# Optimization experiments

Measured on AMD Instinct MI355X. Metric: run time of the kernel, lower is better.

The kernel has to match this reference:

```python
import jax, jax.numpy as jnp
import numpy as np

OFFSETS = jnp.array([[-1, -1], [0, -1], [1, -1], [-1, 0], [0, 0], [1, 0],
                     [-1, 1], [0, 1], [1, 1]], dtype=jnp.float32)  # [9,2]
PIX_STEP = 2.0 / 96.0


def _bilinear_sample(img, gx, gy):
    """Bilinear grid_sample, padding_mode='zeros', align_corners=False.
    img: [B,H,W]; gx, gy: [B,P] in normalized coords [-1,1]. Returns [B,P]."""
    B, H, W = img.shape
    ix = ((gx + 1.0) * W - 1.0) * 0.5  # x indexes width
    iy = ((gy + 1.0) * H - 1.0) * 0.5
    x0f = jnp.floor(ix)
    y0f = jnp.floor(iy)
    wx = ix - x0f
    wy = iy - y0f
    x0 = x0f.astype(jnp.int32)
    y0 = y0f.astype(jnp.int32)
    x1 = x0 + 1
    y1 = y0 + 1
    flat = img.reshape(B, H * W)

    def gather(xi, yi):
        valid = (xi >= 0) & (xi < W) & (yi >= 0) & (yi < H)
        xc = jnp.clip(xi, 0, W - 1)
        yc = jnp.clip(yi, 0, H - 1)
        vals = jnp.take_along_axis(flat, yc * W + xc, axis=1)
        return jnp.where(valid, vals, 0.0)

    v00 = gather(x0, y0)
    v10 = gather(x1, y0)
    v01 = gather(x0, y1)
    v11 = gather(x1, y1)
    return (v00 * (1 - wx) * (1 - wy) + v10 * wx * (1 - wy)
            + v01 * (1 - wx) * wy + v11 * wx * wy)


def setup_inputs() -> dict:
    key = jax.random.key(0)
    k1, k2, k3 = jax.random.split(key, 3)
    B, N, H, W = 256, 16384, 96, 96
    corners = jax.random.uniform(k1, (B, N, 2), dtype=jnp.float32)
    edge_map = jax.random.uniform(k2, (B, 1, H, W), dtype=jnp.float32)
    mask_map = jax.random.uniform(k3, (B, 1, H, W), dtype=jnp.float32)
    return {"corners": corners, "edge_map": edge_map, "mask_map": mask_map}


def reference(corners, edge_map, mask_map):
    B, N, _ = corners.shape
    grid = corners * 2.0 - 1.0  # [B,N,2] (x,y)
    # 9-point neighborhood around each corner: [B,N,9,2]
    neigh = grid[:, :, None, :] + OFFSETS[None, None] * PIX_STEP
    gx = neigh[..., 0].reshape(B, N * 9)
    gy = neigh[..., 1].reshape(B, N * 9)
    sampled_edges = _bilinear_sample(edge_map[:, 0], gx, gy).reshape(B, N, 9)
    best_edge = jnp.max(sampled_edges, axis=-1)  # [B,N]
    edge_align_loss = jnp.mean(1.0 - best_edge)
    sampled_mask = _bilinear_sample(mask_map[:, 0], grid[..., 0], grid[..., 1])  # [B,N]
    mask_align_loss = jnp.mean((sampled_mask - 0.5) ** 2)
    return edge_align_loss + 2.0 * mask_align_loss
```

## Files before the change

kernel.cpp:

```cpp
#include <hip/hip_runtime.h>
#include <hip/hip_fp16.h>

constexpr int Bn = 256;
constexpr int Nn = 16384;
constexpr int Hh = 96;
constexpr int Ww = 96;

constexpr int THREADS = 1024;
constexpr int CHUNKS  = 2;
constexpr int EPS = 100;
constexpr int ESZ = 100 * 100;
constexpr int MPS = 50;
constexpr int MSZ = 100 * 50;
constexpr int PER_THREAD = Nn / CHUNKS / THREADS;

__global__ __launch_bounds__(THREADS, 8)
void geo_kernel(const float* __restrict__ corners,
                const float* __restrict__ edge,
                const float* __restrict__ mask,
                float2* __restrict__ partial)
{
    __shared__ alignas(16) __half2 sE[ESZ];
    __shared__ alignas(16) __half2 sM[MSZ];
    __shared__ float redE[THREADS / 64];
    __shared__ float redM[THREADS / 64];

    const int b     = blockIdx.x >> 1;
    const int chunk = blockIdx.x & 1;
    const int tid   = threadIdx.x;

    const float4* c4 =
        (const float4*)(corners + (size_t)b * Nn * 2 + (size_t)chunk * (Nn / CHUNKS) * 2);
    float4 cc[4];
#pragma unroll
    for (int k = 0; k < 4; ++k)
        cc[k] = c4[k * THREADS + tid];

    {
        const __half2 z2 = __float22half2_rn(make_float2(0.f, 0.f));
        if (tid < 400) sE[(tid < 200) ? tid : (9600 + tid)] = z2;
        if (tid < 288) {
            int r = tid / 3;
            int k = tid - 3 * r;
            int c = (k == 0) ? 0 : (97 + k);
            sE[(r + 2) * EPS + c] = z2;
        }
        if (tid < 200) sM[(tid < 100) ? tid : (4800 + tid)] = z2;
        if (tid < 192) {
            int r = tid >> 1;
            int c = (tid & 1) ? 49 : 0;
            sM[(r + 2) * MPS + c] = z2;
        }
    }

    {
        const float* ebase = edge + (size_t)b * Hh * Ww;
        const float* mbase = mask + (size_t)b * Hh * Ww;
        for (int i = tid; i < Hh * (Ww / 2); i += THREADS) {
            int r = i / (Ww / 2);
            int j = i - r * (Ww / 2);
            const float* erow = ebase + r * Ww;
            float2 ae = *(const float2*)(erow + 2 * j);
            float ne = (2 * j + 2 < Ww) ? erow[2 * j + 2] : 0.f;
            int base = (r + 2) * EPS + 2 * j + 2;
            sE[base]     = __float22half2_rn(make_float2(ae.x, ae.y));
            sE[base + 1] = __float22half2_rn(make_float2(ae.y, ne));
            if (j == 0)
                sE[(r + 2) * EPS + 1] = __float22half2_rn(make_float2(0.f, ae.x));
            float2 am = *(const float2*)(mbase + r * Ww + 2 * j);
            sM[(r + 2) * MPS + 1 + j] = __float22half2_rn(make_float2(am.x, am.y));
        }
    }
    __syncthreads();

    float eAcc = 0.f, mAcc = 0.f;
#pragma unroll
    for (int jj = 0; jj < PER_THREAD; ++jj) {
        float cx = (jj & 1) ? ((jj & 2) ? cc[jj >> 1].z : cc[jj >> 1].z)
                            : cc[jj >> 1].x;
        float cy;
        if (jj & 1) { cx = cc[jj >> 1].z; cy = cc[jj >> 1].w; }
        else        { cx = cc[jj >> 1].x; cy = cc[jj >> 1].y; }
        float ix = fmaf(cx, 96.f, -0.5f);
        float iy = fmaf(cy, 96.f, -0.5f);
        float x0f = floorf(ix), y0f = floorf(iy);
        float wx = ix - x0f, wy = iy - y0f;
        int x0 = (int)x0f, y0 = (int)y0f;

        int cb = (y0 + 1) * EPS + (x0 + 1);
        __half2 e00 = sE[cb],           e01 = sE[cb + 2];
        __half2 e10 = sE[cb + EPS],     e11 = sE[cb + EPS + 2];
        __half2 e20 = sE[cb + 2 * EPS], e21 = sE[cb + 2 * EPS + 2];
        __half2 e30 = sE[cb + 3 * EPS], e31 = sE[cb + 3 * EPS + 2];

        int e0  = (x0 + 2) >> 1;
        int odd = x0 & 1;
        int mb  = (y0 + 2) * MPS + e0;
        __half2 ma_lo = sM[mb],       ma_hi = sM[mb + 1];
        __half2 mc_lo = sM[mb + MPS], mc_hi = sM[mb + MPS + 1];

        float2 r00 = __half22float2(e00), r01 = __half22float2(e01);
        float2 r10 = __half22float2(e10), r11 = __half22float2(e11);
        float2 r20 = __half22float2(e20), r21 = __half22float2(e21);
        float2 r30 = __half22float2(e30), r31 = __half22float2(e31);

        float h[4][3];
        h[0][0] = fmaf(wx, r00.y - r00.x, r00.x);
        h[0][1] = fmaf(wx, r01.x - r00.y, r00.y);
        h[0][2] = fmaf(wx, r01.y - r01.x, r01.x);
        h[1][0] = fmaf(wx, r10.y - r10.x, r10.x);
        h[1][1] = fmaf(wx, r11.x - r10.y, r10.y);
        h[1][2] = fmaf(wx, r11.y - r11.x, r11.x);
        h[2][0] = fmaf(wx, r20.y - r20.x, r20.x);
        h[2][1] = fmaf(wx, r21.x - r20.y, r20.y);
        h[2][2] = fmaf(wx, r21.y - r21.x, r21.x);
        h[3][0] = fmaf(wx, r30.y - r30.x, r30.x);
        h[3][1] = fmaf(wx, r31.x - r30.y, r30.y);
        h[3][2] = fmaf(wx, r31.y - r31.x, r31.x);

        float best = fmaf(wy, h[1][0] - h[0][0], h[0][0]);
#pragma unroll
        for (int r = 0; r < 3; ++r) {
#pragma unroll
            for (int k = 0; k < 3; ++k) {
                if (r == 0 && k == 0) continue;
                float s = fmaf(wy, h[r + 1][k] - h[r][k], h[r][k]);
                best = fmaxf(best, s);
            }
        }
        eAcc += best;

        float2 qa = __half22float2(ma_lo), qb = __half22float2(ma_hi);
        float2 qc = __half22float2(mc_lo), qd = __half22float2(mc_hi);
        float l0 = odd ? qa.y : qa.x;
        float r0 = odd ? qb.x : qa.y;
        float l1 = odd ? qc.y : qc.x;
        float r1 = odd ? qd.x : qc.y;
        float t = fmaf(wx, r0 - l0, l0);
        float u = fmaf(wx, r1 - l1, l1);
        float m = fmaf(wy, u - t, t);
        float d = m - 0.5f;
        mAcc = fmaf(d, d, mAcc);
    }

#pragma unroll
    for (int off = 32; off > 0; off >>= 1) {
        eAcc += __shfl_xor(eAcc, off);
        mAcc += __shfl_xor(mAcc, off);
    }
    const int wv = tid >> 6;
    const int ln = tid & 63;
    if (ln == 0) { redE[wv] = eAcc; redM[wv] = mAcc; }
    __syncthreads();

    if (tid == 0) {
        float e = 0.f, m = 0.f;
#pragma unroll
        for (int w = 0; w < THREADS / 64; ++w) { e += redE[w]; m += redM[w]; }
        partial[blockIdx.x] = make_float2(e, m);
    }
}

__global__ __launch_bounds__(512)
void geo_reduce(const float2* __restrict__ partial, float* __restrict__ out)
{
    __shared__ double rE[8];
    __shared__ double rM[8];
    const int tid = threadIdx.x;
    float2 p = partial[tid];
    double e = (double)p.x, m = (double)p.y;
#pragma unroll
    for (int off = 32; off > 0; off >>= 1) {
        e += __shfl_xor(e, off);
        m += __shfl_xor(m, off);
    }
    if ((tid & 63) == 0) { rE[tid >> 6] = e; rM[tid >> 6] = m; }
    __syncthreads();
    if (tid == 0) {
        double se = 0.0, sm = 0.0;
#pragma unroll
        for (int w = 0; w < 8; ++w) { se += rE[w]; sm += rM[w]; }
        const double inv = 1.0 / (double)((long long)Bn * (long long)Nn);
        double edge_loss = 1.0 - se * inv;
        double mask_loss = sm * inv;
        out[0] = (float)(edge_loss + 2.0 * mask_loss);
    }
}

extern "C" void kernel_launch(void* const* d_in, const int* in_sizes, int n_in,
                              void* d_out, int out_size, void* d_ws, size_t ws_size,
                              hipStream_t stream)
{
    const float* corners = (const float*)d_in[0];
    const float* edge    = (const float*)d_in[1];
    const float* mask    = (const float*)d_in[2];
    float* out      = (float*)d_out;
    float2* partial = (float2*)d_ws;

    geo_kernel<<<Bn * CHUNKS, THREADS, 0, stream>>>(corners, edge, mask, partial);
    geo_reduce<<<1, 512, 0, stream>>>(partial, out);
}
```

Baseline: 28.97 us.

## Halve shared-memory tile via non-duplicated half2 layout and smaller blocks

Replaces the duplicated shifted-pair edge layout (100-wide half2 rows) with a plain packed half2 layout (51 words per row), rebuilding odd-aligned pairs with shift/or funnel operations at sample time. This cuts LDS per block from about 60KB to about 40KB. It also switches to 512-thread blocks with 4 chunks per image, so more blocks can be resident and tile staging overlaps with compute. Corner loads are moved after the barrier and split into two phases. The cost is extra ALU work per sample, staging the image tile twice as often across blocks, and a larger final reduction.

```diff
diff --git a/kernel.cpp b/kernel.cpp
--- a/kernel.cpp
+++ b/kernel.cpp
@@ -6,13 +6,24 @@
 constexpr int Hh = 96;
 constexpr int Ww = 96;
 
-constexpr int THREADS = 1024;
-constexpr int CHUNKS  = 2;
-constexpr int EPS = 100;
-constexpr int ESZ = 100 * 100;
-constexpr int MPS = 50;
-constexpr int MSZ = 100 * 50;
+constexpr int THREADS = 512;
+constexpr int CHUNKS  = 4;
 constexpr int PER_THREAD = Nn / CHUNKS / THREADS;
+
+constexpr int EPS = 51, MPS = 50;
+constexpr int MOFF = 5100;
+constexpr int TOT  = 10000;
+
+static __device__ inline unsigned pack2(float x, float y)
+{
+    __half2 h = __float22half2_rn(make_float2(x, y));
+    return *(unsigned*)&h;
+}
+static __device__ inline float2 unpack2(unsigned u)
+{
+    __half2 h = *(__half2*)&u;
+    return __half22float2(h);
+}
 
 __global__ __launch_bounds__(THREADS, 8)
 void geo_kernel(const float* __restrict__ corners,
@@ -20,127 +31,120 @@
                 const float* __restrict__ mask,
                 float2* __restrict__ partial)
 {
-    __shared__ alignas(16) __half2 sE[ESZ];
-    __shared__ alignas(16) __half2 sM[MSZ];
+    __shared__ unsigned sB[TOT];
     __shared__ float redE[THREADS / 64];
     __shared__ float redM[THREADS / 64];
 
-    const int b     = blockIdx.x >> 1;
-    const int chunk = blockIdx.x & 1;
+    const int b     = blockIdx.x >> 2;
+    const int chunk = blockIdx.x & 3;
     const int tid   = threadIdx.x;
 
-    const float4* c4 =
-        (const float4*)(corners + (size_t)b * Nn * 2 + (size_t)chunk * (Nn / CHUNKS) * 2);
-    float4 cc[4];
-#pragma unroll
-    for (int k = 0; k < 4; ++k)
-        cc[k] = c4[k * THREADS + tid];
-
     {
-        const __half2 z2 = __float22half2_rn(make_float2(0.f, 0.f));
-        if (tid < 400) sE[(tid < 200) ? tid : (9600 + tid)] = z2;
-        if (tid < 288) {
-            int r = tid / 3;
-            int k = tid - 3 * r;
-            int c = (k == 0) ? 0 : (97 + k);
-            sE[(r + 2) * EPS + c] = z2;
-        }
-        if (tid < 200) sM[(tid < 100) ? tid : (4800 + tid)] = z2;
-        if (tid < 192) {
-            int r = tid >> 1;
-            int c = (tid & 1) ? 49 : 0;
-            sM[(r + 2) * MPS + c] = z2;
+        for (int i = tid; i < 784; i += THREADS) {
+            int idx;
+            if (i < 204) {
+                int r = i / 51, c = i - 51 * r;
+                idx = ((r < 2) ? r : (96 + r)) * EPS + c;
+            } else if (i < 492) {
+                int j = i - 204; int r = j / 3; int c3 = j - 3 * r;
+                int c = (c3 == 0) ? 0 : (48 + c3);
+                idx = (r + 2) * EPS + c;
+            } else if (i < 592) {
+                int j = i - 492; int r = (j < 50) ? 0 : 97; int c = j % 50;
+                idx = MOFF + r * MPS + c;
+            } else {
+                int j = i - 592; int r = j >> 1; int c = (j & 1) ? 49 : 0;
+                idx = MOFF + (r + 1) * MPS + c;
+            }
+            sB[idx] = 0u;
         }
     }
 
     {
         const float* ebase = edge + (size_t)b * Hh * Ww;
         const float* mbase = mask + (size_t)b * Hh * Ww;
-        for (int i = tid; i < Hh * (Ww / 2); i += THREADS) {
-            int r = i / (Ww / 2);
-            int j = i - r * (Ww / 2);
-            const float* erow = ebase + r * Ww;
-            float2 ae = *(const float2*)(erow + 2 * j);
-            float ne = (2 * j + 2 < Ww) ? erow[2 * j + 2] : 0.f;
-            int base = (r + 2) * EPS + 2 * j + 2;
-            sE[base]     = __float22half2_rn(make_float2(ae.x, ae.y));
-            sE[base + 1] = __float22half2_rn(make_float2(ae.y, ne));
-            if (j == 0)
-                sE[(r + 2) * EPS + 1] = __float22half2_rn(make_float2(0.f, ae.x));
-            float2 am = *(const float2*)(mbase + r * Ww + 2 * j);
-            sM[(r + 2) * MPS + 1 + j] = __float22half2_rn(make_float2(am.x, am.y));
+        for (int i = tid; i < 2 * 96 * 48; i += THREADS) {
+            int isMask = (i >= 96 * 48);
+            int j = isMask ? (i - 96 * 48) : i;
+            int r = j / 48;
+            int k = j - 48 * r + 1;
+            const float* src = isMask ? mbase : ebase;
+            float2 v = *(const float2*)(src + r * Ww + 2 * k - 2);
+            int idx = isMask ? (MOFF + (r + 1) * MPS + k) : ((r + 2) * EPS + k);
+            sB[idx] = pack2(v.x, v.y);
         }
     }
     __syncthreads();
 
+    const float4* c4 =
+        (const float4*)(corners + (size_t)b * Nn * 2 + (size_t)chunk * (Nn / CHUNKS) * 2);
     float eAcc = 0.f, mAcc = 0.f;
-#pragma unroll
-    for (int jj = 0; jj < PER_THREAD; ++jj) {
-        float cx = (jj & 1) ? ((jj & 2) ? cc[jj >> 1].z : cc[jj >> 1].z)
-                            : cc[jj >> 1].x;
-        float cy;
-        if (jj & 1) { cx = cc[jj >> 1].z; cy = cc[jj >> 1].w; }
-        else        { cx = cc[jj >> 1].x; cy = cc[jj >> 1].y; }
-        float ix = fmaf(cx, 96.f, -0.5f);
-        float iy = fmaf(cy, 96.f, -0.5f);
-        float x0f = floorf(ix), y0f = floorf(iy);
-        float wx = ix - x0f, wy = iy - y0f;
-        int x0 = (int)x0f, y0 = (int)y0f;
-
-        int cb = (y0 + 1) * EPS + (x0 + 1);
-        __half2 e00 = sE[cb],           e01 = sE[cb + 2];
-        __half2 e10 = sE[cb + EPS],     e11 = sE[cb + EPS + 2];
-        __half2 e20 = sE[cb + 2 * EPS], e21 = sE[cb + 2 * EPS + 2];
-        __half2 e30 = sE[cb + 3 * EPS], e31 = sE[cb + 3 * EPS + 2];
-
-        int e0  = (x0 + 2) >> 1;
-        int odd = x0 & 1;
-        int mb  = (y0 + 2) * MPS + e0;
-        __half2 ma_lo = sM[mb],       ma_hi = sM[mb + 1];
-        __half2 mc_lo = sM[mb + MPS], mc_hi = sM[mb + MPS + 1];
-
-        float2 r00 = __half22float2(e00), r01 = __half22float2(e01);
-        float2 r10 = __half22float2(e10), r11 = __half22float2(e11);
-        float2 r20 = __half22float2(e20), r21 = __half22float2(e21);
-        float2 r30 = __half22float2(e30), r31 = __half22float2(e31);
-
-        float h[4][3];
-        h[0][0] = fmaf(wx, r00.y - r00.x, r00.x);
-        h[0][1] = fmaf(wx, r01.x - r00.y, r00.y);
-        h[0][2] = fmaf(wx, r01.y - r01.x, r01.x);
-        h[1][0] = fmaf(wx, r10.y - r10.x, r10.x);
-        h[1][1] = fmaf(wx, r11.x - r10.y, r10.y);
-        h[1][2] = fmaf(wx, r11.y - r11.x, r11.x);
-        h[2][0] = fmaf(wx, r20.y - r20.x, r20.x);
-        h[2][1] = fmaf(wx, r21.x - r20.y, r20.y);
-        h[2][2] = fmaf(wx, r21.y - r21.x, r21.x);
-        h[3][0] = fmaf(wx, r30.y - r30.x, r30.x);
-        h[3][1] = fmaf(wx, r31.x - r30.y, r30.y);
-        h[3][2] = fmaf(wx, r31.y - r31.x, r31.x);
-
-        float best = fmaf(wy, h[1][0] - h[0][0], h[0][0]);
-#pragma unroll
-        for (int r = 0; r < 3; ++r) {
-#pragma unroll
-            for (int k = 0; k < 3; ++k) {
-                if (r == 0 && k == 0) continue;
-                float s = fmaf(wy, h[r + 1][k] - h[r][k], h[r][k]);
-                best = fmaxf(best, s);
+
+#pragma unroll
+    for (int ph = 0; ph < 2; ++ph) {
+        float4 ca = c4[(2 * ph + 0) * THREADS + tid];
+        float4 cb = c4[(2 * ph + 1) * THREADS + tid];
+#pragma unroll
+        for (int jj = 0; jj < 4; ++jj) {
+            float cx, cy;
+            if      (jj == 0) { cx = ca.x; cy = ca.y; }
+            else if (jj == 1) { cx = ca.z; cy = ca.w; }
+            else if (jj == 2) { cx = cb.x; cy = cb.y; }
+            else              { cx = cb.z; cy = cb.w; }
+
+            float ix = fmaf(cx, 96.f, -0.5f);
+            float iy = fmaf(cy, 96.f, -0.5f);
+            float x0f = floorf(ix), y0f = floorf(iy);
+            float wx = ix - x0f, wy = iy - y0f;
+            int x0 = (int)x0f, y0 = (int)y0f;
+
+            int pe = x0 + 1;
+            int s  = pe & 1;
+            int e0 = pe >> 1;
+            int rb = (y0 + 1) * EPS + e0;
+
+            float h[4][3];
+#pragma unroll
+            for (int rr = 0; rr < 4; ++rr) {
+                int base = rb + rr * EPS;
+                unsigned u0 = sB[base];
+                unsigned u1 = sB[base + 1];
+                unsigned u2 = sB[base + 2];
+                unsigned w0 = s ? ((u0 >> 16) | (u1 << 16)) : u0;
+                unsigned w1 = s ? ((u1 >> 16) | (u2 << 16)) : u1;
+                float2 f01 = unpack2(w0);
+                float2 f23 = unpack2(w1);
+                h[rr][0] = fmaf(wx, f01.y - f01.x, f01.x);
+                h[rr][1] = fmaf(wx, f23.x - f01.y, f01.y);
+                h[rr][2] = fmaf(wx, f23.y - f23.x, f23.x);
             }
+            float best = fmaf(wy, h[1][0] - h[0][0], h[0][0]);
+#pragma unroll
+            for (int r = 0; r < 3; ++r)
+#pragma unroll
+                for (int k = 0; k < 3; ++k) {
+                    if (r == 0 && k == 0) continue;
+                    float v = fmaf(wy, h[r + 1][k] - h[r][k], h[r][k]);
+                    best = fmaxf(best, v);
+                }
+            eAcc += best;
+
+            int pm  = x0 + 2;
+            int sm  = pm & 1;
+            int em  = pm >> 1;
+            int mb  = MOFF + (y0 + 1) * MPS + em;
+            unsigned m0 = sB[mb],       m1 = sB[mb + 1];
+            unsigned m2 = sB[mb + MPS], m3 = sB[mb + MPS + 1];
+            unsigned wt = sm ? ((m0 >> 16) | (m1 << 16)) : m0;
+            unsigned wb = sm ? ((m2 >> 16) | (m3 << 16)) : m2;
+            float2 ft = unpack2(wt);
+            float2 fb = unpack2(wb);
+            float t = fmaf(wx, ft.y - ft.x, ft.x);
+            float u = fmaf(wx, fb.y - fb.x, fb.x);
+            float m = fmaf(wy, u - t, t);
+            float d = m - 0.5f;
+            mAcc = fmaf(d, d, mAcc);
         }
-        eAcc += best;
-
-        float2 qa = __half22float2(ma_lo), qb = __half22float2(ma_hi);
-        float2 qc = __half22float2(mc_lo), qd = __half22float2(mc_hi);
-        float l0 = odd ? qa.y : qa.x;
-        float r0 = odd ? qb.x : qa.y;
-        float l1 = odd ? qc.y : qc.x;
-        float r1 = odd ? qd.x : qc.y;
-        float t = fmaf(wx, r0 - l0, l0);
-        float u = fmaf(wx, r1 - l1, l1);
-        float m = fmaf(wy, u - t, t);
-        float d = m - 0.5f;
-        mAcc = fmaf(d, d, mAcc);
     }
 
 #pragma unroll
@@ -161,11 +165,11 @@
     }
 }
 
-__global__ __launch_bounds__(512)
+__global__ __launch_bounds__(1024)
 void geo_reduce(const float2* __restrict__ partial, float* __restrict__ out)
 {
-    __shared__ double rE[8];
-    __shared__ double rM[8];
+    __shared__ double rE[16];
+    __shared__ double rM[16];
     const int tid = threadIdx.x;
     float2 p = partial[tid];
     double e = (double)p.x, m = (double)p.y;
@@ -179,7 +183,7 @@
     if (tid == 0) {
         double se = 0.0, sm = 0.0;
 #pragma unroll
-        for (int w = 0; w < 8; ++w) { se += rE[w]; sm += rM[w]; }
+        for (int w = 0; w < 16; ++w) { se += rE[w]; sm += rM[w]; }
         const double inv = 1.0 / (double)((long long)Bn * (long long)Nn);
         double edge_loss = 1.0 - se * inv;
         double mask_loss = sm * inv;
@@ -198,5 +202,5 @@
     float2* partial = (float2*)d_ws;
 
     geo_kernel<<<Bn * CHUNKS, THREADS, 0, stream>>>(corners, edge, mask, partial);
-    geo_reduce<<<1, 512, 0, stream>>>(partial, out);
-}
+    geo_reduce<<<1, 1024, 0, stream>>>(partial, out);
+}
```

After: 88.33 us. 3.05x slower.
